# Optimization experiments

Measured on AMD Instinct MI355X. Metric: run time of the kernel, lower is better.

## Reference

```python
import jax, jax.numpy as jnp
import numpy as np

B = 1024          # number of graphs
N = 64            # atoms per graph
NUM_NODES = B * N
HID = 256         # hidden_channels
H1 = HID // 2
E = 2_097_152     # edges (avg degree 32)


def _xavier(k, fan_in, fan_out):
    lim = np.sqrt(6.0 / (fan_in + fan_out)).astype(np.float32)
    return jax.random.uniform(k, (fan_in, fan_out), jnp.float32, -lim, lim)


def setup_inputs() -> dict:
    key = jax.random.key(0)
    ks = jax.random.split(key, 6)
    node_features = jax.random.normal(ks[0], (NUM_NODES, HID), jnp.float32)
    edge_index = jax.random.randint(ks[1], (2, E), 0, NUM_NODES)
    batch = jnp.repeat(jnp.arange(B), N)  # sorted graph ids, equal-size graphs
    W1 = _xavier(ks[2], HID + 1, H1); b1 = jnp.zeros((H1,), jnp.float32)
    W2 = _xavier(ks[3], H1, H1);      b2 = jnp.zeros((H1,), jnp.float32)
    W3 = _xavier(ks[4], H1, 1);       b3 = jnp.zeros((1,), jnp.float32)
    kT = jnp.ones((1,), jnp.float32)
    return {"node_features": node_features, "W1": W1, "b1": b1, "W2": W2,
            "b2": b2, "W3": W3, "b3": b3, "kT": kT,
            "edge_index": edge_index, "batch": batch}


def reference(node_features, W1, b1, W2, b2, W3, b3, kT, edge_index, batch):
    num_nodes = node_features.shape[0]
    # node degree: count of occurrences as source node
    deg = jnp.zeros((num_nodes,), jnp.float32).at[edge_index[0]].add(1.0)
    # per-graph atom counts and segment start offsets (n_atoms_i)
    counts = jax.ops.segment_sum(jnp.ones((num_nodes,), jnp.float32), batch,
                                 num_segments=B)
    start = jnp.cumsum(counts) - counts  # exclusive cumsum
    # stable per-graph sort of degrees in one shot: lexsort keys, primary=batch
    order = jnp.lexsort((deg, batch))  # global original indices, sorted by (batch, deg)
    # connectivity feature: local original index of the k-th smallest-degree
    # node in its graph, normalized by graph size (matches sorted_index / n_atoms_i)
    conn = (order.astype(jnp.float32) - start[batch]) / counts[batch]
    # MLP(hidden+1 -> hid/2 -> hid/2 -> 1) with silu
    x = jnp.concatenate([conn[:, None], node_features], axis=-1)  # [nodes, HID+1]
    h = jax.nn.silu(x @ W1 + b1)
    h = jax.nn.silu(h @ W2 + b2)
    logits = (h @ W3 + b3)[:, 0] / kT[0]
    # per-graph (segment) softmax
    m = jax.ops.segment_max(logits, batch, num_segments=B)
    e = jnp.exp(logits - m[batch])
    s = jax.ops.segment_sum(e, batch, num_segments=B)
    return e / s[batch]  # concat of per-graph softmaxed probabilities
```

## Files before the change

### kernel.cpp

```cpp
#include <hip/hip_runtime.h>

#define NB 1024
#define NPG 64
#define NUM_NODES 65536
#define HID 256
#define H1DIM 128
#define NE 2097152

typedef __attribute__((ext_vector_type(8))) _Float16 f16x8;
typedef __attribute__((ext_vector_type(4))) float f32x4;

#define W2F_HALF 32768
#define PART_OFF (128*1024)

__global__ __launch_bounds__(256) void prep_hist_kernel(
    const float* __restrict__ W1, const float* __restrict__ W2,
    _Float16* __restrict__ wf,
    const int4* __restrict__ src4, unsigned int* __restrict__ partials, int G)
{
    __shared__ unsigned int h[16384];
    const int bx = blockIdx.x;
    const int t = threadIdx.x;

    if (bx < 96) {
        const int L = t & 63;
        const int j2 = (t >> 6) * 2;
        const float* src;
        _Float16* dst;
        int kt, nt;
        if (bx < 64) { kt = bx >> 3; nt = bx & 7; src = W1 + H1DIM; dst = wf + bx * 512; }
        else { int bb = bx - 64; kt = bb >> 3; nt = bb & 7; src = W2; dst = wf + W2F_HALF + bb * 512; }
        const int k = kt * 32 + (L >> 4) * 8 + j2;
        const int n = nt * 16 + (L & 15);
        dst[L * 8 + j2]     = (_Float16)src[k * H1DIM + n];
        dst[L * 8 + j2 + 1] = (_Float16)src[(k + 1) * H1DIM + n];
        return;
    }

    const int b = bx - 96;
    uint4* h4 = (uint4*)h;
    for (int i = t; i < 4096; i += 256) h4[i] = make_uint4(0u, 0u, 0u, 0u);
    __syncthreads();
    const int n4 = (NE / 4) / G;
    const int4* p = src4 + b * n4;
    for (int i = t; i < n4; i += 256) {
        int4 v = p[i];
        atomicAdd(&h[v.x >> 2], 1u << ((v.x & 3) * 8));
        atomicAdd(&h[v.y >> 2], 1u << ((v.y & 3) * 8));
        atomicAdd(&h[v.z >> 2], 1u << ((v.z & 3) * 8));
        atomicAdd(&h[v.w >> 2], 1u << ((v.w & 3) * 8));
    }
    __syncthreads();
    uint4* dst = (uint4*)(partials + b * 16384);
    for (int i = t; i < 4096; i += 256) dst[i] = h4[i];
}

__global__ __launch_bounds__(256, 4) void mlp_softmax_kernel(
    const float* __restrict__ feat,
    const float* __restrict__ W1, const float* __restrict__ b1,
    const float* __restrict__ b2,
    const float* __restrict__ W3, const float* __restrict__ b3,
    const float* __restrict__ kT,
    const _Float16* __restrict__ wf,
    const unsigned int* __restrict__ partials, int G,
    float* __restrict__ out)
{
    __shared__ _Float16 h1f[4][4][64][8];
    __shared__ unsigned int dpart[16][16];
    __shared__ unsigned int degs[NPG];
    __shared__ float conns[NPG];
    __shared__ float logits_s[NPG];

    const int tid = threadIdx.x;
    const int L = tid & 63;
    const int w = __builtin_amdgcn_readfirstlane(tid >> 6);
    const int q = L >> 4;
    const int c = L & 15;
    const int g = blockIdx.x;
    const int node0 = g * NPG;

    const int wd = tid & 15, sg = tid >> 4;
    const int ns = G >> 4;
    unsigned int dtmp[16];
    const unsigned int* dp = partials + (size_t)(sg * ns) * 16384 + g * 16 + wd;
#pragma unroll
    for (int i = 0; i < 16; ++i) dtmp[i] = (i < ns) ? dp[(size_t)i * 16384] : 0u;

    const float* featw = &feat[(size_t)(node0 + w * 16 + c) * HID + q * 8];
    float4 fa[8], fb[8];
#pragma unroll
    for (int kt = 0; kt < 8; ++kt) {
        fa[kt] = *(const float4*)(featw + kt * 32);
        fb[kt] = *(const float4*)(featw + kt * 32 + 4);
    }
    float b1v[8], w1r0[8];
#pragma unroll
    for (int nt = 0; nt < 8; ++nt) {
        b1v[nt]  = b1[nt * 16 + c];
        w1r0[nt] = W1[nt * 16 + c];
    }

    unsigned int dsum = 0;
#pragma unroll
    for (int i = 0; i < 16; ++i) dsum += dtmp[i];
    dpart[sg][wd] = dsum;
    __syncthreads();
    if (tid < 16) {
        unsigned int s = 0;
#pragma unroll
        for (int k = 0; k < 16; ++k) s += dpart[k][tid];
        degs[tid * 4 + 0] = s & 255u;
        degs[tid * 4 + 1] = (s >> 8) & 255u;
        degs[tid * 4 + 2] = (s >> 16) & 255u;
        degs[tid * 4 + 3] = s >> 24;
    }
    __syncthreads();
    if (tid < NPG) {
        unsigned int di = degs[tid];
        int rk = 0;
#pragma unroll 8
        for (int j = 0; j < NPG; ++j) {
            unsigned int dj = degs[j];
            rk += (int)((dj < di) | ((dj == di) & (j < tid)));
        }
        conns[rk] = (float)tid * (1.0f / 64.0f);
    }
    __syncthreads();

    f16x8 af[8];
#pragma unroll
    for (int kt = 0; kt < 8; ++kt) {
        float4 A = fa[kt], B = fb[kt];
        f16x8 v = { (_Float16)A.x, (_Float16)A.y, (_Float16)A.z, (_Float16)A.w,
                    (_Float16)B.x, (_Float16)B.y, (_Float16)B.z, (_Float16)B.w };
        af[kt] = v;
    }

    float cn[4];
#pragma unroll
    for (int r = 0; r < 4; ++r) cn[r] = conns[w * 16 + q * 4 + r];
    f32x4 acc[8];
#pragma unroll
    for (int nt = 0; nt < 8; ++nt)
#pragma unroll
        for (int r = 0; r < 4; ++r)
            acc[nt][r] = fmaf(cn[r], w1r0[nt], b1v[nt]);

#pragma unroll
    for (int kt = 0; kt < 8; ++kt) {
#pragma unroll
        for (int nt = 0; nt < 8; ++nt) {
            f16x8 bfv = *(const f16x8*)&wf[(kt * 8 + nt) * 512 + L * 8];
            acc[nt] = __builtin_amdgcn_mfma_f32_16x16x32_f16(af[kt], bfv, acc[nt], 0, 0, 0);
        }
    }

    float b2v[8], w3v[8];
#pragma unroll
    for (int nt = 0; nt < 8; ++nt) {
        b2v[nt] = b2[nt * 16 + c];
        w3v[nt] = W3[nt * 16 + c];
    }

#pragma unroll
    for (int nt = 0; nt < 8; ++nt) {
        const int ktp = nt >> 1;
        const int lp = (((nt & 1) << 1) + (c >> 3)) * 16 + q * 4;
        const int j = c & 7;
#pragma unroll
        for (int r = 0; r < 4; ++r) {
            float v = acc[nt][r];
            float hv = v / (1.0f + __expf(-v));
            h1f[w][ktp][lp + r][j] = (_Float16)hv;
        }
    }

    f32x4 acc2[8];
#pragma unroll
    for (int nt = 0; nt < 8; ++nt)
#pragma unroll
        for (int r = 0; r < 4; ++r) acc2[nt][r] = b2v[nt];
    const _Float16* w2f = wf + W2F_HALF;
#pragma unroll
    for (int kt = 0; kt < 4; ++kt) {
        f16x8 a = *(const f16x8*)&h1f[w][kt][L][0];
#pragma unroll
        for (int nt = 0; nt < 8; ++nt) {
            f16x8 bfv = *(const f16x8*)&w2f[(kt * 8 + nt) * 512 + L * 8];
            acc2[nt] = __builtin_amdgcn_mfma_f32_16x16x32_f16(a, bfv, acc2[nt], 0, 0, 0);
        }
    }

    float lg[4] = {0.0f, 0.0f, 0.0f, 0.0f};
#pragma unroll
    for (int nt = 0; nt < 8; ++nt)
#pragma unroll
        for (int r = 0; r < 4; ++r) {
            float v = acc2[nt][r];
            float hv = v / (1.0f + __expf(-v));
            lg[r] = fmaf(hv, w3v[nt], lg[r]);
        }
#pragma unroll
    for (int d = 1; d < 16; d <<= 1)
#pragma unroll
        for (int r = 0; r < 4; ++r) lg[r] += __shfl_xor(lg[r], d, 64);
    if (c == 0) {
#pragma unroll
        for (int r = 0; r < 4; ++r) logits_s[w * 16 + q * 4 + r] = lg[r];
    }
    __syncthreads();

    if (tid < NPG) {
        float s = (logits_s[tid] + b3[0]) / kT[0];
        float m = s;
#pragma unroll
        for (int d = 1; d < 64; d <<= 1) m = fmaxf(m, __shfl_xor(m, d, 64));
        float e = __expf(s - m);
        float su = e;
#pragma unroll
        for (int d = 1; d < 64; d <<= 1) su += __shfl_xor(su, d, 64);
        out[node0 + tid] = e / su;
    }
}

extern "C" void kernel_launch(void* const* d_in, const int* in_sizes, int n_in,
                              void* d_out, int out_size, void* d_ws, size_t ws_size,
                              hipStream_t stream)
{
    const float* feat = (const float*)d_in[0];
    const float* W1   = (const float*)d_in[1];
    const float* b1   = (const float*)d_in[2];
    const float* W2   = (const float*)d_in[3];
    const float* b2   = (const float*)d_in[4];
    const float* W3   = (const float*)d_in[5];
    const float* b3   = (const float*)d_in[6];
    const float* kT   = (const float*)d_in[7];
    const int*   ei   = (const int*)d_in[8];

    float* out = (float*)d_out;
    _Float16* wf = (_Float16*)d_ws;
    unsigned int* partials = (unsigned int*)((char*)d_ws + PART_OFF);

    int G = 256;
    while (G > 16 && ws_size < (size_t)PART_OFF + (size_t)G * 65536) G >>= 1;

    prep_hist_kernel<<<96 + G, 256, 0, stream>>>(W1, W2, wf, (const int4*)ei,
                                                 partials, G);
    mlp_softmax_kernel<<<NB, 256, 0, stream>>>(feat, W1, b1, b2, W3, b3, kT,
                                               wf, partials, G, out);
}
```

Measured before the change: 145.0 us.

## Stage fp16 weights in LDS and add a separate degree-reduction kernel

Degree partials are now summed by a new small kernel into a per-node degree array, instead of each MLP block reading 16-way strided partials. The histogram split drops from 256 to 64 slices. Each MLP block copies the W1 then W2 fp16 fragments into a 64KB shared buffer and runs MFMA on those instead of global memory, reusing the buffer for the h1 tile. The cost is an extra kernel launch, two more block barriers, and launch bounds lowered to 2 blocks per CU because of the larger LDS footprint.

```diff
diff --git a/kernel.cpp b/kernel.cpp
--- a/kernel.cpp
+++ b/kernel.cpp
@@ -10,8 +10,8 @@
 typedef __attribute__((ext_vector_type(8))) _Float16 f16x8;
 typedef __attribute__((ext_vector_type(4))) float f32x4;
 
-#define W2F_HALF 32768
-#define PART_OFF (128*1024)
+#define DEGF_OFF (128*1024)
+#define PART_OFF (192*1024)
 
 __global__ __launch_bounds__(256) void prep_hist_kernel(
     const float* __restrict__ W1, const float* __restrict__ W2,
@@ -29,7 +29,7 @@
         _Float16* dst;
         int kt, nt;
         if (bx < 64) { kt = bx >> 3; nt = bx & 7; src = W1 + H1DIM; dst = wf + bx * 512; }
-        else { int bb = bx - 64; kt = bb >> 3; nt = bb & 7; src = W2; dst = wf + W2F_HALF + bb * 512; }
+        else { int bb = bx - 64; kt = bb >> 3; nt = bb & 7; src = W2; dst = wf + 32768 + bb * 512; }
         const int k = kt * 32 + (L >> 4) * 8 + j2;
         const int n = nt * 16 + (L & 15);
         dst[L * 8 + j2]     = (_Float16)src[k * H1DIM + n];
@@ -55,18 +55,38 @@
     for (int i = t; i < 4096; i += 256) dst[i] = h4[i];
 }
 
-__global__ __launch_bounds__(256, 4) void mlp_softmax_kernel(
+__global__ __launch_bounds__(256) void dreduce_kernel(
+    const unsigned int* __restrict__ partials,
+    unsigned int* __restrict__ degf, int G)
+{
+    const int i = blockIdx.x * 256 + threadIdx.x;
+    unsigned int a0 = 0, a1 = 0, a2 = 0, a3 = 0, a4 = 0, a5 = 0, a6 = 0, a7 = 0;
+    for (int sl = 0; sl < G; sl += 8) {
+        a0 += partials[(sl + 0) * 16384 + i];
+        a1 += partials[(sl + 1) * 16384 + i];
+        a2 += partials[(sl + 2) * 16384 + i];
+        a3 += partials[(sl + 3) * 16384 + i];
+        a4 += partials[(sl + 4) * 16384 + i];
+        a5 += partials[(sl + 5) * 16384 + i];
+        a6 += partials[(sl + 6) * 16384 + i];
+        a7 += partials[(sl + 7) * 16384 + i];
+    }
+    unsigned int s = ((a0 + a1) + (a2 + a3)) + ((a4 + a5) + (a6 + a7));
+    *(uint4*)&degf[i * 4] = make_uint4(s & 255u, (s >> 8) & 255u,
+                                       (s >> 16) & 255u, s >> 24);
+}
+
+__global__ __launch_bounds__(256, 2) void mlp_softmax_kernel(
     const float* __restrict__ feat,
     const float* __restrict__ W1, const float* __restrict__ b1,
     const float* __restrict__ b2,
     const float* __restrict__ W3, const float* __restrict__ b3,
     const float* __restrict__ kT,
     const _Float16* __restrict__ wf,
-    const unsigned int* __restrict__ partials, int G,
+    const unsigned int* __restrict__ degf,
     float* __restrict__ out)
 {
-    __shared__ _Float16 h1f[4][4][64][8];
-    __shared__ unsigned int dpart[16][16];
+    __shared__ _Float16 wfs[32768];
     __shared__ unsigned int degs[NPG];
     __shared__ float conns[NPG];
     __shared__ float logits_s[NPG];
@@ -79,12 +99,18 @@
     const int g = blockIdx.x;
     const int node0 = g * NPG;
 
-    const int wd = tid & 15, sg = tid >> 4;
-    const int ns = G >> 4;
-    unsigned int dtmp[16];
-    const unsigned int* dp = partials + (size_t)(sg * ns) * 16384 + g * 16 + wd;
-#pragma unroll
-    for (int i = 0; i < 16; ++i) dtmp[i] = (i < ns) ? dp[(size_t)i * 16384] : 0u;
+#pragma unroll
+    for (int rb = 0; rb < 2; ++rb) {
+        f16x8 t[8];
+#pragma unroll
+        for (int i = 0; i < 8; ++i)
+            t[i] = *(const f16x8*)&wf[((rb * 8 + i) * 256 + tid) * 8];
+#pragma unroll
+        for (int i = 0; i < 8; ++i)
+            *(f16x8*)&wfs[((rb * 8 + i) * 256 + tid) * 8] = t[i];
+    }
+
+    if (tid < NPG) degs[tid] = degf[node0 + tid];
 
     const float* featw = &feat[(size_t)(node0 + w * 16 + c) * HID + q * 8];
     float4 fa[8], fb[8];
@@ -93,27 +119,15 @@
         fa[kt] = *(const float4*)(featw + kt * 32);
         fb[kt] = *(const float4*)(featw + kt * 32 + 4);
     }
-    float b1v[8], w1r0[8];
+    float b1v[8], w1r0[8], b2v[8], w3v[8];
 #pragma unroll
     for (int nt = 0; nt < 8; ++nt) {
         b1v[nt]  = b1[nt * 16 + c];
         w1r0[nt] = W1[nt * 16 + c];
-    }
-
-    unsigned int dsum = 0;
-#pragma unroll
-    for (int i = 0; i < 16; ++i) dsum += dtmp[i];
-    dpart[sg][wd] = dsum;
-    __syncthreads();
-    if (tid < 16) {
-        unsigned int s = 0;
-#pragma unroll
-        for (int k = 0; k < 16; ++k) s += dpart[k][tid];
-        degs[tid * 4 + 0] = s & 255u;
-        degs[tid * 4 + 1] = (s >> 8) & 255u;
-        degs[tid * 4 + 2] = (s >> 16) & 255u;
-        degs[tid * 4 + 3] = s >> 24;
-    }
+        b2v[nt]  = b2[nt * 16 + c];
+        w3v[nt]  = W3[nt * 16 + c];
+    }
+
     __syncthreads();
     if (tid < NPG) {
         unsigned int di = degs[tid];
@@ -150,16 +164,21 @@
     for (int kt = 0; kt < 8; ++kt) {
 #pragma unroll
         for (int nt = 0; nt < 8; ++nt) {
-            f16x8 bfv = *(const f16x8*)&wf[(kt * 8 + nt) * 512 + L * 8];
+            f16x8 bfv = *(const f16x8*)&wfs[(kt * 8 + nt) * 512 + L * 8];
             acc[nt] = __builtin_amdgcn_mfma_f32_16x16x32_f16(af[kt], bfv, acc[nt], 0, 0, 0);
         }
     }
 
-    float b2v[8], w3v[8];
-#pragma unroll
-    for (int nt = 0; nt < 8; ++nt) {
-        b2v[nt] = b2[nt * 16 + c];
-        w3v[nt] = W3[nt * 16 + c];
+    __syncthreads();
+
+    {
+        f16x8 t[8];
+#pragma unroll
+        for (int i = 0; i < 8; ++i)
+            t[i] = *(const f16x8*)&wf[32768 + (i * 256 + tid) * 8];
+#pragma unroll
+        for (int i = 0; i < 8; ++i)
+            *(f16x8*)&wfs[(i * 256 + tid) * 8] = t[i];
     }
 
 #pragma unroll
@@ -171,22 +190,22 @@
         for (int r = 0; r < 4; ++r) {
             float v = acc[nt][r];
             float hv = v / (1.0f + __expf(-v));
-            h1f[w][ktp][lp + r][j] = (_Float16)hv;
-        }
-    }
+            wfs[16384 + w * 2048 + ktp * 512 + (lp + r) * 8 + j] = (_Float16)hv;
+        }
+    }
+    __syncthreads();
 
     f32x4 acc2[8];
 #pragma unroll
     for (int nt = 0; nt < 8; ++nt)
 #pragma unroll
         for (int r = 0; r < 4; ++r) acc2[nt][r] = b2v[nt];
-    const _Float16* w2f = wf + W2F_HALF;
 #pragma unroll
     for (int kt = 0; kt < 4; ++kt) {
-        f16x8 a = *(const f16x8*)&h1f[w][kt][L][0];
+        f16x8 a = *(const f16x8*)&wfs[16384 + w * 2048 + kt * 512 + L * 8];
 #pragma unroll
         for (int nt = 0; nt < 8; ++nt) {
-            f16x8 bfv = *(const f16x8*)&w2f[(kt * 8 + nt) * 512 + L * 8];
+            f16x8 bfv = *(const f16x8*)&wfs[(kt * 8 + nt) * 512 + L * 8];
             acc2[nt] = __builtin_amdgcn_mfma_f32_16x16x32_f16(a, bfv, acc2[nt], 0, 0, 0);
         }
     }
@@ -239,13 +258,15 @@
 
     float* out = (float*)d_out;
     _Float16* wf = (_Float16*)d_ws;
+    unsigned int* degf = (unsigned int*)((char*)d_ws + DEGF_OFF);
     unsigned int* partials = (unsigned int*)((char*)d_ws + PART_OFF);
 
-    int G = 256;
-    while (G > 16 && ws_size < (size_t)PART_OFF + (size_t)G * 65536) G >>= 1;
+    int G = 64;
+    while (G > 8 && ws_size < (size_t)PART_OFF + (size_t)G * 65536) G >>= 1;
 
     prep_hist_kernel<<<96 + G, 256, 0, stream>>>(W1, W2, wf, (const int4*)ei,
                                                  partials, G);
+    dreduce_kernel<<<64, 256, 0, stream>>>(partials, degf, G);
     mlp_softmax_kernel<<<NB, 256, 0, stream>>>(feat, W1, b1, b2, W3, b3, kT,
-                                               wf, partials, G, out);
-}
+                                               wf, degf, out);
+}
```

Result: no change. 147.5 us (+1.7%).

## Stage MLP weights in LDS via async DMA, two graphs per block

Applied to the files above, without the earlier changes.

The MLP kernel now handles two graphs per 512-thread block. It copies the f16 W1 and then W2 fragment tiles into a 64KB shared buffer with global_load_lds instead of reading them from global memory for every MFMA, and reuses that buffer for the h1 intermediate. The histogram grid is fixed at 128 partial blocks, which halves the number of partials each graph must sum, and its loops are unrolled. This costs extra __syncthreads, heavy LDS use that limits occupancy, and drops the fallback that shrank the grid when workspace is small.

```diff
diff --git a/kernel.cpp b/kernel.cpp
--- a/kernel.cpp
+++ b/kernel.cpp
@@ -6,17 +6,23 @@
 #define HID 256
 #define H1DIM 128
 #define NE 2097152
+#define GH 128
 
 typedef __attribute__((ext_vector_type(8))) _Float16 f16x8;
 typedef __attribute__((ext_vector_type(4))) float f32x4;
 
-#define W2F_HALF 32768
 #define PART_OFF (128*1024)
+
+__device__ __forceinline__ void dma16(const void* g, void* l) {
+    __builtin_amdgcn_global_load_lds(
+        (const __attribute__((address_space(1))) unsigned int*)g,
+        (__attribute__((address_space(3))) unsigned int*)l, 16, 0, 0);
+}
 
 __global__ __launch_bounds__(256) void prep_hist_kernel(
     const float* __restrict__ W1, const float* __restrict__ W2,
     _Float16* __restrict__ wf,
-    const int4* __restrict__ src4, unsigned int* __restrict__ partials, int G)
+    const int4* __restrict__ src4, unsigned int* __restrict__ partials)
 {
     __shared__ unsigned int h[16384];
     const int bx = blockIdx.x;
@@ -29,7 +35,7 @@
         _Float16* dst;
         int kt, nt;
         if (bx < 64) { kt = bx >> 3; nt = bx & 7; src = W1 + H1DIM; dst = wf + bx * 512; }
-        else { int bb = bx - 64; kt = bb >> 3; nt = bb & 7; src = W2; dst = wf + W2F_HALF + bb * 512; }
+        else { int bb = bx - 64; kt = bb >> 3; nt = bb & 7; src = W2; dst = wf + 32768 + bb * 512; }
         const int k = kt * 32 + (L >> 4) * 8 + j2;
         const int n = nt * 16 + (L & 15);
         dst[L * 8 + j2]     = (_Float16)src[k * H1DIM + n];
@@ -39,11 +45,12 @@
 
     const int b = bx - 96;
     uint4* h4 = (uint4*)h;
-    for (int i = t; i < 4096; i += 256) h4[i] = make_uint4(0u, 0u, 0u, 0u);
-    __syncthreads();
-    const int n4 = (NE / 4) / G;
-    const int4* p = src4 + b * n4;
-    for (int i = t; i < n4; i += 256) {
+#pragma unroll
+    for (int i = 0; i < 16; ++i) h4[t + i * 256] = make_uint4(0u, 0u, 0u, 0u);
+    __syncthreads();
+    const int4* p = src4 + b * ((NE / 4) / GH);
+#pragma unroll 4
+    for (int i = t; i < (NE / 4) / GH; i += 256) {
         int4 v = p[i];
         atomicAdd(&h[v.x >> 2], 1u << ((v.x & 3) * 8));
         atomicAdd(&h[v.y >> 2], 1u << ((v.y & 3) * 8));
@@ -52,41 +59,51 @@
     }
     __syncthreads();
     uint4* dst = (uint4*)(partials + b * 16384);
-    for (int i = t; i < 4096; i += 256) dst[i] = h4[i];
-}
-
-__global__ __launch_bounds__(256, 4) void mlp_softmax_kernel(
+#pragma unroll
+    for (int i = 0; i < 16; ++i) dst[t + i * 256] = h4[t + i * 256];
+}
+
+__global__ __launch_bounds__(512, 4) void mlp_softmax_kernel(
     const float* __restrict__ feat,
     const float* __restrict__ W1, const float* __restrict__ b1,
     const float* __restrict__ b2,
     const float* __restrict__ W3, const float* __restrict__ b3,
     const float* __restrict__ kT,
     const _Float16* __restrict__ wf,
-    const unsigned int* __restrict__ partials, int G,
+    const unsigned int* __restrict__ partials,
     float* __restrict__ out)
 {
-    __shared__ _Float16 h1f[4][4][64][8];
-    __shared__ unsigned int dpart[16][16];
-    __shared__ unsigned int degs[NPG];
-    __shared__ float conns[NPG];
-    __shared__ float logits_s[NPG];
+    __shared__ _Float16 wfs[32768];
+    __shared__ unsigned int dpart[2][16][16];
+    __shared__ unsigned int degs[2][NPG];
+    __shared__ float conns[2][NPG];
+    __shared__ float logits_s[2][NPG];
 
     const int tid = threadIdx.x;
     const int L = tid & 63;
     const int w = __builtin_amdgcn_readfirstlane(tid >> 6);
+    const int h = w >> 2;
+    const int w4 = w & 3;
     const int q = L >> 4;
     const int c = L & 15;
-    const int g = blockIdx.x;
-    const int node0 = g * NPG;
-
-    const int wd = tid & 15, sg = tid >> 4;
-    const int ns = G >> 4;
-    unsigned int dtmp[16];
-    const unsigned int* dp = partials + (size_t)(sg * ns) * 16384 + g * 16 + wd;
-#pragma unroll
-    for (int i = 0; i < 16; ++i) dtmp[i] = (i < ns) ? dp[(size_t)i * 16384] : 0u;
-
-    const float* featw = &feat[(size_t)(node0 + w * 16 + c) * HID + q * 8];
+    const int g0 = blockIdx.x * 2;
+    const int node0 = g0 * NPG;
+
+#pragma unroll
+    for (int i = 0; i < 8; ++i)
+        dma16(&wf[(i * 512 + tid) * 8], &wfs[(i * 512 + w * 64) * 8]);
+
+    {
+        const int t256 = tid & 255;
+        const int wd = t256 & 15, sg = t256 >> 4;
+        const unsigned int* p = partials + (size_t)(sg * 8) * 16384 + (g0 + h) * 16 + wd;
+        unsigned int s = 0;
+#pragma unroll
+        for (int i = 0; i < 8; ++i) s += p[(size_t)i * 16384];
+        dpart[h][sg][wd] = s;
+    }
+
+    const float* featw = &feat[(size_t)(node0 + h * 64 + w4 * 16 + c) * HID + q * 8];
     float4 fa[8], fb[8];
 #pragma unroll
     for (int kt = 0; kt < 8; ++kt) {
@@ -100,30 +117,28 @@
         w1r0[nt] = W1[nt * 16 + c];
     }
 
-    unsigned int dsum = 0;
-#pragma unroll
-    for (int i = 0; i < 16; ++i) dsum += dtmp[i];
-    dpart[sg][wd] = dsum;
-    __syncthreads();
-    if (tid < 16) {
+    __syncthreads();
+    if (tid < 32) {
+        const int hh = tid >> 4, wd = tid & 15;
         unsigned int s = 0;
 #pragma unroll
-        for (int k = 0; k < 16; ++k) s += dpart[k][tid];
-        degs[tid * 4 + 0] = s & 255u;
-        degs[tid * 4 + 1] = (s >> 8) & 255u;
-        degs[tid * 4 + 2] = (s >> 16) & 255u;
-        degs[tid * 4 + 3] = s >> 24;
-    }
-    __syncthreads();
-    if (tid < NPG) {
-        unsigned int di = degs[tid];
+        for (int k = 0; k < 16; ++k) s += dpart[hh][k][wd];
+        degs[hh][wd * 4 + 0] = s & 255u;
+        degs[hh][wd * 4 + 1] = (s >> 8) & 255u;
+        degs[hh][wd * 4 + 2] = (s >> 16) & 255u;
+        degs[hh][wd * 4 + 3] = s >> 24;
+    }
+    __syncthreads();
+    if ((tid & 192) == 0) {
+        const int hh = tid >> 8, i = tid & 63;
+        unsigned int di = degs[hh][i];
         int rk = 0;
 #pragma unroll 8
         for (int j = 0; j < NPG; ++j) {
-            unsigned int dj = degs[j];
-            rk += (int)((dj < di) | ((dj == di) & (j < tid)));
-        }
-        conns[rk] = (float)tid * (1.0f / 64.0f);
+            unsigned int dj = degs[hh][j];
+            rk += (int)((dj < di) | ((dj == di) & (j < i)));
+        }
+        conns[hh][rk] = (float)i * (1.0f / 64.0f);
     }
     __syncthreads();
 
@@ -138,7 +153,7 @@
 
     float cn[4];
 #pragma unroll
-    for (int r = 0; r < 4; ++r) cn[r] = conns[w * 16 + q * 4 + r];
+    for (int r = 0; r < 4; ++r) cn[r] = conns[h][w4 * 16 + q * 4 + r];
     f32x4 acc[8];
 #pragma unroll
     for (int nt = 0; nt < 8; ++nt)
@@ -150,17 +165,16 @@
     for (int kt = 0; kt < 8; ++kt) {
 #pragma unroll
         for (int nt = 0; nt < 8; ++nt) {
-            f16x8 bfv = *(const f16x8*)&wf[(kt * 8 + nt) * 512 + L * 8];
+            f16x8 bfv = *(const f16x8*)&wfs[(kt * 8 + nt) * 512 + L * 8];
             acc[nt] = __builtin_amdgcn_mfma_f32_16x16x32_f16(af[kt], bfv, acc[nt], 0, 0, 0);
         }
     }
 
-    float b2v[8], w3v[8];
-#pragma unroll
-    for (int nt = 0; nt < 8; ++nt) {
-        b2v[nt] = b2[nt * 16 + c];
-        w3v[nt] = W3[nt * 16 + c];
-    }
+    __syncthreads();
+
+#pragma unroll
+    for (int i = 0; i < 4; ++i)
+        dma16(&wf[32768 + (i * 512 + tid) * 8], &wfs[(i * 512 + w * 64) * 8]);
 
 #pragma unroll
     for (int nt = 0; nt < 8; ++nt) {
@@ -171,22 +185,28 @@
         for (int r = 0; r < 4; ++r) {
             float v = acc[nt][r];
             float hv = v / (1.0f + __expf(-v));
-            h1f[w][ktp][lp + r][j] = (_Float16)hv;
-        }
-    }
+            wfs[16384 + w * 2048 + ktp * 512 + (lp + r) * 8 + j] = (_Float16)hv;
+        }
+    }
+    float b2v[8], w3v[8];
+#pragma unroll
+    for (int nt = 0; nt < 8; ++nt) {
+        b2v[nt] = b2[nt * 16 + c];
+        w3v[nt] = W3[nt * 16 + c];
+    }
+    __syncthreads();
 
     f32x4 acc2[8];
 #pragma unroll
     for (int nt = 0; nt < 8; ++nt)
 #pragma unroll
         for (int r = 0; r < 4; ++r) acc2[nt][r] = b2v[nt];
-    const _Float16* w2f = wf + W2F_HALF;
 #pragma unroll
     for (int kt = 0; kt < 4; ++kt) {
-        f16x8 a = *(const f16x8*)&h1f[w][kt][L][0];
+        f16x8 a = *(const f16x8*)&wfs[16384 + w * 2048 + kt * 512 + L * 8];
 #pragma unroll
         for (int nt = 0; nt < 8; ++nt) {
-            f16x8 bfv = *(const f16x8*)&w2f[(kt * 8 + nt) * 512 + L * 8];
+            f16x8 bfv = *(const f16x8*)&wfs[(kt * 8 + nt) * 512 + L * 8];
             acc2[nt] = __builtin_amdgcn_mfma_f32_16x16x32_f16(a, bfv, acc2[nt], 0, 0, 0);
         }
     }
@@ -206,12 +226,13 @@
         for (int r = 0; r < 4; ++r) lg[r] += __shfl_xor(lg[r], d, 64);
     if (c == 0) {
 #pragma unroll
-        for (int r = 0; r < 4; ++r) logits_s[w * 16 + q * 4 + r] = lg[r];
-    }
-    __syncthreads();
-
-    if (tid < NPG) {
-        float s = (logits_s[tid] + b3[0]) / kT[0];
+        for (int r = 0; r < 4; ++r) logits_s[h][w4 * 16 + q * 4 + r] = lg[r];
+    }
+    __syncthreads();
+
+    if ((tid & 192) == 0) {
+        const int hh = tid >> 8, i = tid & 63;
+        float s = (logits_s[hh][i] + b3[0]) / kT[0];
         float m = s;
 #pragma unroll
         for (int d = 1; d < 64; d <<= 1) m = fmaxf(m, __shfl_xor(m, d, 64));
@@ -219,7 +240,7 @@
         float su = e;
 #pragma unroll
         for (int d = 1; d < 64; d <<= 1) su += __shfl_xor(su, d, 64);
-        out[node0 + tid] = e / su;
+        out[node0 + hh * NPG + i] = e / su;
     }
 }
 
@@ -241,11 +262,8 @@
     _Float16* wf = (_Float16*)d_ws;
     unsigned int* partials = (unsigned int*)((char*)d_ws + PART_OFF);
 
-    int G = 256;
-    while (G > 16 && ws_size < (size_t)PART_OFF + (size_t)G * 65536) G >>= 1;
-
-    prep_hist_kernel<<<96 + G, 256, 0, stream>>>(W1, W2, wf, (const int4*)ei,
-                                                 partials, G);
-    mlp_softmax_kernel<<<NB, 256, 0, stream>>>(feat, W1, b1, b2, W3, b3, kT,
-                                               wf, partials, G, out);
-}
+    prep_hist_kernel<<<96 + GH, 256, 0, stream>>>(W1, W2, wf, (const int4*)ei,
+                                                  partials);
+    mlp_softmax_kernel<<<NB / 2, 512, 0, stream>>>(feat, W1, b1, b2, W3, b3,
+                                                   kT, wf, partials, out);
+}
```

After: 135.9 us. 6.3% less time.
